# Performance work log

Hardware: AMD Instinct MI355X
Metric: run time of the kernel (lower is better)

The kernel has to match this reference:

```python
import jax, jax.numpy as jnp
import numpy as np
import math

B, C, N, T = 8, 128, 256, 64  # batch, d_model, nodes, timesteps
H = 8                          # attention heads
NUM_STEPS = 50                 # diffusion steps


def _conv2d(x, w, b):
    # Conv2d with kernel (1,3), padding (0,1); x: (B,C,N,T), w: (O,I,1,3)
    y = jax.lax.conv_general_dilated(x, w, (1, 1), [(0, 0), (1, 1)],
                                     dimension_numbers=('NCHW', 'OIHW', 'NCHW'))
    return y + b[None, :, None, None]


def _linear(x, w, b=None):
    y = jnp.einsum('...i,oi->...o', x, w)
    return y if b is None else y + b


def _ln(x, g, b, eps=1e-5):
    m = jnp.mean(x, -1, keepdims=True)
    v = jnp.var(x, -1, keepdims=True)
    return (x - m) * jax.lax.rsqrt(v + eps) * g + b


def _forward(step, x, adj, wq, bq, wk, bk, w1, b1, w2, b2, theta,
             ln0_g, ln0_b, ln1_g, ln1_b, p1_w, p1_b, p2_w, p2_b,
             dxc_w, dxc_b, dec_w, dec_b, dc1_w, dc1_b, dp2_w, dp2_b):
    dk = C // H
    sq = 1.0 / math.sqrt(dk)
    sc = 1.0 / math.sqrt(C)
    # ---- normalized graph Laplacian: D^{-1/2} A D^{-1/2} (get_laplacian, normalize=True)
    d = jnp.sum(adj, -1) ** -0.5
    Lap = adj * d[:, None] * d[None, :]  # (N,N)
    # ---- temporal attention with conv-derived Q/K (MultiHeadAttentionAwareTemporal)
    q = _conv2d(x, wq, bq).reshape(B, H, dk, N, T).transpose(0, 3, 1, 4, 2)  # (B,N,H,T,dk)
    k = _conv2d(x, wk, bk).reshape(B, H, dk, N, T).transpose(0, 3, 1, 4, 2)
    v = _linear(x.transpose(0, 2, 3, 1), w1, b1).reshape(B, N, T, H, dk).transpose(0, 1, 3, 2, 4)
    p = jax.nn.softmax(jnp.einsum('bnhtd,bnhsd->bnhts', q, k) * sq, axis=-1)
    o = jnp.einsum('bnhts,bnhsd->bnhtd', p, v).transpose(0, 1, 3, 2, 4).reshape(B, N, T, C)
    xp = x.transpose(0, 2, 3, 1) + _ln(_linear(o, w2, b2), ln0_g, ln0_b)  # (B,N,T,C)
    # ---- spatial attention GCN (Spatial_Attention_layer + spatialAttentionGCN)
    xt = xp.transpose(0, 2, 1, 3)  # (B,T,N,C)
    sat = jax.nn.softmax(jnp.einsum('btnf,btmf->btnm', xt, xt) * sc, axis=-1) * sc
    y = jnp.einsum('btnm,btmf->btnf', Lap[None, None] * sat, xt)
    y = jax.nn.relu(_linear(y, theta)).transpose(0, 2, 1, 3)  # (B,N,T,C)
    h = xp + _ln(y, ln1_g, ln1_b)
    # ---- diffusion step embedding (DiffusionEmbedding)
    dim = C // 2
    freqs = 10.0 ** (jnp.arange(dim, dtype=jnp.float32) / (dim - 1) * 4.0)
    tab = jnp.arange(NUM_STEPS, dtype=jnp.float32)[:, None] * freqs[None, :]
    tab = jnp.concatenate([jnp.sin(tab), jnp.cos(tab)], -1)  # (NUM_STEPS, C)
    e = jax.nn.silu(_linear(tab[step], p1_w, p1_b))
    e = jax.nn.silu(_linear(e, p2_w, p2_b))  # (B,C)
    h = h + e[:, None, None, :]
    # ---- Decoder: conv + sigmoid-gated add + relu + 1x1 projection to 2 channels
    enc = h.transpose(0, 3, 1, 2)  # (B,C,N,T)
    xh = _conv2d(enc, dxc_w, dxc_b)
    ec = _conv2d(enc, dec_w, dec_b)
    out = jax.nn.relu(xh + jax.nn.sigmoid(ec) + _conv2d(ec, dc1_w, dc1_b))
    out = jnp.einsum('bcnt,oc->bont', out, dp2_w) + dp2_b[None, :, None, None]  # (B,2,N,T)
    return out


def setup_inputs() -> dict:
    key = jax.random.key(0)
    ks = iter(jax.random.split(key, 40))
    s = 1.0 / math.sqrt(C)
    sk = 1.0 / math.sqrt(3 * C)

    def nrm(shape, scale):
        return jax.random.normal(next(ks), shape, jnp.float32) * scale

    return {
        'x': nrm((B, C, N, T), 1.0),
        'adj': jax.random.uniform(next(ks), (N, N), jnp.float32, 0.1, 1.0),
        'step': jax.random.randint(next(ks), (B,), 0, NUM_STEPS, jnp.int32),
        'wq': nrm((C, C, 1, 3), sk), 'bq': jnp.zeros((C,), jnp.float32),
        'wk': nrm((C, C, 1, 3), sk), 'bk': jnp.zeros((C,), jnp.float32),
        'w1': nrm((C, C), s), 'b1': jnp.zeros((C,), jnp.float32),
        'w2': nrm((C, C), s), 'b2': jnp.zeros((C,), jnp.float32),
        'theta': nrm((C, C), s),
        'ln0_g': jnp.ones((C,), jnp.float32), 'ln0_b': jnp.zeros((C,), jnp.float32),
        'ln1_g': jnp.ones((C,), jnp.float32), 'ln1_b': jnp.zeros((C,), jnp.float32),
        'p1_w': nrm((C, C), s), 'p1_b': jnp.zeros((C,), jnp.float32),
        'p2_w': nrm((C, C), s), 'p2_b': jnp.zeros((C,), jnp.float32),
        'dxc_w': nrm((C, C, 1, 3), sk), 'dxc_b': jnp.zeros((C,), jnp.float32),
        'dec_w': nrm((C, C, 1, 3), sk), 'dec_b': jnp.zeros((C,), jnp.float32),
        'dc1_w': nrm((C, C, 1, 3), sk), 'dc1_b': jnp.zeros((C,), jnp.float32),
        'dp2_w': nrm((2, C), s), 'dp2_b': jnp.zeros((2,), jnp.float32),
    }


def reference(x, adj, step, wq, bq, wk, bk, w1, b1, w2, b2, theta,
              ln0_g, ln0_b, ln1_g, ln1_b, p1_w, p1_b, p2_w, p2_b,
              dxc_w, dxc_b, dec_w, dec_b, dc1_w, dc1_b, dp2_w, dp2_b):
    return _forward(step, x, adj, wq, bq, wk, bk, w1, b1, w2, b2, theta,
                    ln0_g, ln0_b, ln1_g, ln1_b, p1_w, p1_b, p2_w, p2_b,
                    dxc_w, dxc_b, dec_w, dec_b, dc1_w, dc1_b, dp2_w, dp2_b)
```

## Files before the change

### kernel.cpp

```cpp
#include <hip/hip_runtime.h>
#include <hip/hip_bf16.h>

namespace {

constexpr int C = 128, N = 256, T = 64, Bsz = 8;
constexpr int TILE = T * C;
constexpr size_t BIGE = (size_t)Bsz * N * T * C;

typedef short v8s __attribute__((ext_vector_type(8)));
typedef float v4f __attribute__((ext_vector_type(4)));

__device__ __forceinline__ float bfu(unsigned short u) {
  unsigned int x = ((unsigned int)u) << 16;
  return __uint_as_float(x);
}
__device__ __forceinline__ unsigned short f2b(float v) {
  __hip_bfloat16 h = __float2bfloat16(v);
  return *(unsigned short*)&h;
}
__device__ __forceinline__ unsigned int pk2(float a, float b) {
  return (unsigned int)f2b(a) | ((unsigned int)f2b(b) << 16);
}
__device__ __forceinline__ float ld(const void* p, size_t i, int f32) {
  if (f32) return ((const float*)p)[i];
  return bfu(((const unsigned short*)p)[i]);
}
__device__ __forceinline__ float sigm(float x) { return 1.f / (1.f + __expf(-x)); }

__global__ __launch_bounds__(64) void k_sniff(const unsigned short* x, int* flag) {
  __shared__ int cnt[64];
  int tid = threadIdx.x;
  int c = 0;
  for (int u = 0; u < 8; ++u) {
    unsigned short v = x[tid * 8 + u];
    int e = (v >> 7) & 255;
    c += (e >= 97 && e <= 157) ? 1 : 0;
  }
  cnt[tid] = c;
  __syncthreads();
  if (tid == 0) {
    int s = 0;
    for (int i = 0; i < 64; ++i) s += cnt[i];
    flag[0] = (s < 435) ? 1 : 0;
  }
}

struct PrepArgs {
  const int* flag;
  const void *wq, *wk, *w1, *w2, *th, *dxc, *dec, *dc1;
  const void *bq, *bk, *b1, *b2, *l0g, *l0b, *l1g, *l1b, *dxcb, *decb, *dc1b, *dp2w, *dp2b;
  unsigned short *wqkB, *w1B, *w2B;
  __hip_bfloat16* thB;
  unsigned short *decWb, *dxcWb, *dc1Wb;
  float *bqk, *b1f, *b2f, *l0gf, *l0bf, *l1gf, *l1bf, *dxcbf, *decbf, *dc1bf, *dp2wf, *dp2bf;
};

__global__ __launch_bounds__(256) void k_prep(PrepArgs a) {
  int f = a.flag[0];
  int idx = blockIdx.x * blockDim.x + threadIdx.x;
  int stride = gridDim.x * blockDim.x;
  for (int i = idx; i < 256 * 384; i += stride) {
    int o = i / 384, k = i - o * 384;
    int j = k >> 7, ii = k & 127;
    float v = (o < 128) ? ld(a.wq, (o * 128 + ii) * 3 + j, f)
                        : ld(a.wk, ((o - 128) * 128 + ii) * 3 + j, f);
    a.wqkB[i] = f2b(v);
  }
  for (int i = idx; i < 16384; i += stride) {
    a.w1B[i] = f2b(ld(a.w1, i, f));
    a.w2B[i] = f2b(ld(a.w2, i, f));
    a.thB[i] = __float2bfloat16(ld(a.th, i, f));
  }
  for (int i = idx; i < 16384; i += stride) {
    int o = i >> 7, ii = i & 127;
    int sbase = (o * 128 + ii) * 3;
#pragma unroll
    for (int j = 0; j < 3; ++j) {
      int dsti = o * 384 + j * 128 + ii;
      a.decWb[dsti] = f2b(ld(a.dec, sbase + j, f));
      a.dxcWb[dsti] = f2b(ld(a.dxc, sbase + j, f));
      a.dc1Wb[dsti] = f2b(ld(a.dc1, sbase + j, f));
    }
  }
  for (int i = idx; i < 256; i += stride) {
    a.bqk[i] = (i < 128) ? ld(a.bq, i, f) : ld(a.bk, i - 128, f);
    a.dp2wf[i] = ld(a.dp2w, i, f);
  }
  for (int i = idx; i < 128; i += stride) {
    a.b1f[i] = ld(a.b1, i, f);   a.b2f[i] = ld(a.b2, i, f);
    a.l0gf[i] = ld(a.l0g, i, f); a.l0bf[i] = ld(a.l0b, i, f);
    a.l1gf[i] = ld(a.l1g, i, f); a.l1bf[i] = ld(a.l1b, i, f);
    a.dxcbf[i] = ld(a.dxcb, i, f); a.decbf[i] = ld(a.decb, i, f); a.dc1bf[i] = ld(a.dc1b, i, f);
  }
  if (idx < 2) a.dp2bf[idx] = ld(a.dp2b, idx, f);
}

__global__ __launch_bounds__(256) void k_lap(const void* adj, const int* flag, float* lap) {
  __shared__ float dsh[256];
  int f = flag[0];
  int tid = threadIdx.x;
  float s = 0.f;
  for (int m = 0; m < 256; ++m) s += ld(adj, tid * 256 + m, f);
  dsh[tid] = 1.f / sqrtf(s);
  __syncthreads();
  for (int idx = tid; idx < 65536; idx += 256) {
    int n = idx >> 8, m = idx & 255;
    lap[idx] = ld(adj, idx, f) * dsh[n] * dsh[m];
  }
}

__global__ __launch_bounds__(128) void k_emb(const int* step, const int* flag,
                                             const void* p1w, const void* p1b,
                                             const void* p2w, const void* p2b, float* e) {
  int b = blockIdx.x, c = threadIdx.x;
  int f = flag[0];
  __shared__ float tab[128], e1[128];
  float sv = (float)step[b];
  int i0 = c & 63;
  float fr = powf(10.f, (float)i0 / 63.f * 4.f);
  float ang = sv * fr;
  tab[c] = (c < 64) ? sinf(ang) : cosf(ang);
  __syncthreads();
  float a = ld(p1b, c, f);
  for (int i = 0; i < 128; ++i) a += tab[i] * ld(p1w, c * 128 + i, f);
  a = a * sigm(a);
  e1[c] = a;
  __syncthreads();
  float a2 = ld(p2b, c, f);
  for (int i = 0; i < 128; ++i) a2 += e1[i] * ld(p2w, c * 128 + i, f);
  e[b * 128 + c] = a2 * sigm(a2);
}

constexpr int XBS = 136;
constexpr int VTS = 72;

__global__ __launch_bounds__(512, 4) void k_mega1(
    const void* xin, const int* flag,
    const unsigned short* wqkB, const float* bqk,
    const unsigned short* w1B, const float* b1f,
    const unsigned short* w2B, const float* b2f,
    const float* l0g, const float* l0b, float* g0) {
  int bn = blockIdx.x, b = bn >> 8, n = bn & 255;
  __shared__ unsigned short Xb[66 * XBS];
  __shared__ unsigned short qo[64 * XBS];
  __shared__ unsigned short kls[64 * XBS];
  __shared__ unsigned short vT[128 * VTS];
  __shared__ float pS[8 * 64], pQ[8 * 64];
  __shared__ float mrow[64], vrow[64];
  int tid = threadIdx.x;
  int wv = tid >> 6, lane = tid & 63, quad = lane >> 4, lr = lane & 15;
  int f = flag[0];
  int hb = wv * 16;
  const v8s zz = {0, 0, 0, 0, 0, 0, 0, 0};
  {
    size_t xoff = (size_t)b * C * N * T + (size_t)n * T;
    for (int idx = tid * 4; idx < TILE; idx += 2048) {
      int i = idx >> 6, t = idx & 63;
      unsigned short pk[4];
      if (f) {
        float4 v4 = *(const float4*)&((const float*)xin)[xoff + (size_t)i * N * T + t];
        pk[0] = f2b(v4.x); pk[1] = f2b(v4.y); pk[2] = f2b(v4.z); pk[3] = f2b(v4.w);
      } else {
        ushort4 u4 = *(const ushort4*)&((const unsigned short*)xin)[xoff + (size_t)i * N * T + t];
        pk[0] = u4.x; pk[1] = u4.y; pk[2] = u4.z; pk[3] = u4.w;
      }
#pragma unroll
      for (int u = 0; u < 4; ++u) Xb[(t + u + 1) * XBS + i] = pk[u];
    }
    if (tid < 128) { Xb[tid] = 0; Xb[65 * XBS + tid] = 0; }
  }
  __syncthreads();
  {
    int mt0 = wv * 2;
    v4f acc[2][4];
#pragma unroll
    for (int mi = 0; mi < 2; ++mi)
#pragma unroll
      for (int nt = 0; nt < 4; ++nt) acc[mi][nt] = (v4f){0.f, 0.f, 0.f, 0.f};
    for (int j = 0; j < 3; ++j) {
#pragma unroll
      for (int kt = 0; kt < 4; ++kt) {
        int ko = j * 128 + kt * 32 + quad * 8;
        v8s a0 = *(const v8s*)&wqkB[(mt0 * 16 + lr) * 384 + ko];
        v8s a1 = *(const v8s*)&wqkB[((mt0 + 1) * 16 + lr) * 384 + ko];
        int bko = kt * 32 + quad * 8;
#pragma unroll
        for (int nt = 0; nt < 4; ++nt) {
          v8s bb = *(const v8s*)&Xb[(nt * 16 + lr + j) * XBS + bko];
          acc[0][nt] = __builtin_amdgcn_mfma_f32_16x16x32_bf16(a0, bb, acc[0][nt], 0, 0, 0);
          acc[1][nt] = __builtin_amdgcn_mfma_f32_16x16x32_bf16(a1, bb, acc[1][nt], 0, 0, 0);
        }
      }
    }
    unsigned short* dst = (wv < 4) ? qo : kls;
#pragma unroll
    for (int mi = 0; mi < 2; ++mi) {
      int og = (mt0 + mi) * 16 + quad * 4;
      int oo = og & 127;
#pragma unroll
      for (int nt = 0; nt < 4; ++nt) {
        int t = nt * 16 + lr;
        *(unsigned int*)&dst[t * XBS + oo] =
            pk2(acc[mi][nt][0] + bqk[og], acc[mi][nt][1] + bqk[og + 1]);
        *(unsigned int*)&dst[t * XBS + oo + 2] =
            pk2(acc[mi][nt][2] + bqk[og + 2], acc[mi][nt][3] + bqk[og + 3]);
      }
    }
  }
  {
    v4f av[4];
#pragma unroll
    for (int nt = 0; nt < 4; ++nt) av[nt] = (v4f){0.f, 0.f, 0.f, 0.f};
#pragma unroll
    for (int kt = 0; kt < 4; ++kt) {
      int ko = kt * 32 + quad * 8;
      v8s a = *(const v8s*)&w1B[(wv * 16 + lr) * 128 + ko];
#pragma unroll
      for (int nt = 0; nt < 4; ++nt) {
        v8s bb = *(const v8s*)&Xb[(nt * 16 + lr + 1) * XBS + ko];
        av[nt] = __builtin_amdgcn_mfma_f32_16x16x32_bf16(a, bb, av[nt], 0, 0, 0);
      }
    }
#pragma unroll
    for (int nt = 0; nt < 4; ++nt) {
      int t = nt * 16 + lr;
#pragma unroll
      for (int r = 0; r < 4; ++r) {
        int o = hb + quad * 4 + r;
        vT[o * VTS + t] = f2b(av[nt][r] + b1f[o]);
      }
    }
  }
  __syncthreads();
  {
    v4f sa[4][4];
#pragma unroll
    for (int ms = 0; ms < 4; ++ms)
#pragma unroll
      for (int nt = 0; nt < 4; ++nt) sa[ms][nt] = (v4f){0.f, 0.f, 0.f, 0.f};
    {
      v8s afs[4], bfs[4];
#pragma unroll
      for (int ms = 0; ms < 4; ++ms)
        afs[ms] = (quad < 2) ? *(const v8s*)&kls[(ms * 16 + lr) * XBS + hb + quad * 8] : zz;
#pragma unroll
      for (int nt = 0; nt < 4; ++nt)
        bfs[nt] = (quad < 2) ? *(const v8s*)&qo[(nt * 16 + lr) * XBS + hb + quad * 8] : zz;
#pragma unroll
      for (int ms = 0; ms < 4; ++ms)
#pragma unroll
        for (int nt = 0; nt < 4; ++nt)
          sa[ms][nt] = __builtin_amdgcn_mfma_f32_16x16x32_bf16(afs[ms], bfs[nt], sa[ms][nt], 0, 0, 0);
    }
#pragma unroll
    for (int nt = 0; nt < 4; ++nt) {
      float mx = -1e30f;
#pragma unroll
      for (int ms = 0; ms < 4; ++ms)
#pragma unroll
        for (int r = 0; r < 4; ++r) {
          float v = sa[ms][nt][r] * 0.25f;
          sa[ms][nt][r] = v;
          mx = fmaxf(mx, v);
        }
      mx = fmaxf(mx, __shfl_xor(mx, 16, 64));
      mx = fmaxf(mx, __shfl_xor(mx, 32, 64));
      float ssum = 0.f;
#pragma unroll
      for (int ms = 0; ms < 4; ++ms)
#pragma unroll
        for (int r = 0; r < 4; ++r) {
          float e = __expf(sa[ms][nt][r] - mx);
          sa[ms][nt][r] = e;
          ssum += e;
        }
      ssum += __shfl_xor(ssum, 16, 64);
      ssum += __shfl_xor(ssum, 32, 64);
      float inv = 1.f / ssum;
#pragma unroll
      for (int ms = 0; ms < 4; ++ms)
#pragma unroll
        for (int r = 0; r < 4; ++r) sa[ms][nt][r] *= inv;
    }
    v4f ov[4];
#pragma unroll
    for (int nt = 0; nt < 4; ++nt) ov[nt] = (v4f){0.f, 0.f, 0.f, 0.f};
#pragma unroll
    for (int kt = 0; kt < 2; ++kt) {
      unsigned int pA[4][2], pB[4][2];
#pragma unroll
      for (int nt = 0; nt < 4; ++nt) {
#pragma unroll
        for (int h = 0; h < 2; ++h) {
          pA[nt][h] = pk2(sa[2 * kt][nt][2 * h], sa[2 * kt][nt][2 * h + 1]);
          pB[nt][h] = pk2(sa[2 * kt + 1][nt][2 * h], sa[2 * kt + 1][nt][2 * h + 1]);
        }
      }
      v8s aV = *(const v8s*)&vT[(hb + lr) * VTS + kt * 32 + quad * 8];
#pragma unroll
      for (int nt = 0; nt < 4; ++nt) {
        union { unsigned int u[4]; v8s s; } bu;
#pragma unroll
        for (int w = 0; w < 4; ++w) {
          int src = (2 * (quad & 1) + (w >> 1)) * 16 + lr;
          unsigned int x0 = (unsigned int)__shfl((int)pA[nt][w & 1], src, 64);
          unsigned int x1 = (unsigned int)__shfl((int)pB[nt][w & 1], src, 64);
          bu.u[w] = (quad >> 1) ? x1 : x0;
        }
        ov[nt] = __builtin_amdgcn_mfma_f32_16x16x32_bf16(aV, bu.s, ov[nt], 0, 0, 0);
      }
    }
#pragma unroll
    for (int nt = 0; nt < 4; ++nt) {
      int t = nt * 16 + lr;
      *(unsigned int*)&qo[t * XBS + hb + quad * 4] = pk2(ov[nt][0], ov[nt][1]);
      *(unsigned int*)&qo[t * XBS + hb + quad * 4 + 2] = pk2(ov[nt][2], ov[nt][3]);
    }
  }
  __syncthreads();
  v4f aw[4];
  {
#pragma unroll
    for (int nt = 0; nt < 4; ++nt) aw[nt] = (v4f){0.f, 0.f, 0.f, 0.f};
#pragma unroll
    for (int kt = 0; kt < 4; ++kt) {
      int ko = kt * 32 + quad * 8;
      v8s a = *(const v8s*)&w2B[(wv * 16 + lr) * 128 + ko];
#pragma unroll
      for (int nt = 0; nt < 4; ++nt) {
        v8s bb = *(const v8s*)&qo[(nt * 16 + lr) * XBS + ko];
        aw[nt] = __builtin_amdgcn_mfma_f32_16x16x32_bf16(a, bb, aw[nt], 0, 0, 0);
      }
    }
    int ob = hb + quad * 4;
#pragma unroll
    for (int nt = 0; nt < 4; ++nt) {
      float s = 0.f, q2 = 0.f;
#pragma unroll
      for (int r = 0; r < 4; ++r) {
        aw[nt][r] += b2f[ob + r];
        s += aw[nt][r];
        q2 += aw[nt][r] * aw[nt][r];
      }
      s += __shfl_xor(s, 16, 64);  s += __shfl_xor(s, 32, 64);
      q2 += __shfl_xor(q2, 16, 64); q2 += __shfl_xor(q2, 32, 64);
      if (quad == 0) {
        pS[wv * 64 + nt * 16 + lr] = s;
        pQ[wv * 64 + nt * 16 + lr] = q2;
      }
    }
  }
  __syncthreads();
  if (tid < 64) {
    float s = 0.f, q2 = 0.f;
#pragma unroll
    for (int w = 0; w < 8; ++w) { s += pS[w * 64 + tid]; q2 += pQ[w * 64 + tid]; }
    float mm = s * (1.f / 128.f);
    mrow[tid] = mm;
    vrow[tid] = rsqrtf(q2 * (1.f / 128.f) - mm * mm + 1e-5f);
  }
  __syncthreads();
  {
    int ob = hb + quad * 4;
    float gg[4], bb2[4];
#pragma unroll
    for (int r = 0; r < 4; ++r) { gg[r] = l0g[ob + r]; bb2[r] = l0b[ob + r]; }
    float* dst = g0 + (size_t)bn * TILE;
#pragma unroll
    for (int nt = 0; nt < 4; ++nt) {
      int t = nt * 16 + lr;
      float m = mrow[t], rs = vrow[t];
      ushort4 xr = *(const ushort4*)&Xb[(t + 1) * XBS + ob];
      float4 o4;
      o4.x = (aw[nt][0] - m) * rs * gg[0] + bb2[0] + bfu(xr.x);
      o4.y = (aw[nt][1] - m) * rs * gg[1] + bb2[1] + bfu(xr.y);
      o4.z = (aw[nt][2] - m) * rs * gg[2] + bb2[2] + bfu(xr.z);
      o4.w = (aw[nt][3] - m) * rs * gg[3] + bb2[3] + bfu(xr.w);
      *(float4*)&dst[t * 128 + ob] = o4;
    }
  }
}

constexpr int XS = 136;
constexpr int TS = 264;

__global__ __launch_bounds__(512, 1) void k_megasp(
    const float* g0, const float* lap, float* yout) {
  int bt = blockIdx.x, b = bt >> 6, t = bt & 63;
  __shared__ unsigned short Xhi[256 * XS];
  __shared__ unsigned short Xlo[256 * XS];
  unsigned short* Xt = Xlo;
  unsigned short* Pld = Xhi;
  int tid = threadIdx.x;
  int wv = tid >> 6, lane = tid & 63, quad = lane >> 4, lr = lane & 15;
  int wrow0 = wv * 32;
  const float sc = 0.08838834764831845f;
  {
    size_t base = (size_t)b * (N * (size_t)TILE) + (size_t)t * 128;
    for (int idx = tid * 4; idx < 32768; idx += 2048) {
      int n = idx >> 7, c = idx & 127;
      float4 v4 = *(const float4*)&g0[base + (size_t)n * TILE + c];
      ushort4 h, l;
      h.x = f2b(v4.x); l.x = f2b(v4.x - bfu(h.x));
      h.y = f2b(v4.y); l.y = f2b(v4.y - bfu(h.y));
      h.z = f2b(v4.z); l.z = f2b(v4.z - bfu(h.z));
      h.w = f2b(v4.w); l.w = f2b(v4.w - bfu(h.w));
      *(ushort4*)&Xhi[n * XS + c] = h;
      *(ushort4*)&Xlo[n * XS + c] = l;
    }
  }
  __syncthreads();
  v4f acc[2][16];
#pragma unroll
  for (int mi = 0; mi < 2; ++mi)
#pragma unroll
    for (int nt = 0; nt < 16; ++nt) acc[mi][nt] = (v4f){0.f, 0.f, 0.f, 0.f};
  for (int kt = 0; kt < 4; ++kt) {
    int ko = kt * 32 + quad * 8;
    v8s ah0 = *(const v8s*)&Xhi[(wrow0 + lr) * XS + ko];
    v8s al0 = *(const v8s*)&Xlo[(wrow0 + lr) * XS + ko];
    v8s ah1 = *(const v8s*)&Xhi[(wrow0 + 16 + lr) * XS + ko];
    v8s al1 = *(const v8s*)&Xlo[(wrow0 + 16 + lr) * XS + ko];
#pragma unroll
    for (int nt = 0; nt < 16; ++nt) {
      v8s bh = *(const v8s*)&Xhi[(nt * 16 + lr) * XS + ko];
      v8s bl = *(const v8s*)&Xlo[(nt * 16 + lr) * XS + ko];
      acc[0][nt] = __builtin_amdgcn_mfma_f32_16x16x32_bf16(ah0, bh, acc[0][nt], 0, 0, 0);
      acc[0][nt] = __builtin_amdgcn_mfma_f32_16x16x32_bf16(ah0, bl, acc[0][nt], 0, 0, 0);
      acc[0][nt] = __builtin_amdgcn_mfma_f32_16x16x32_bf16(al0, bh, acc[0][nt], 0, 0, 0);
      acc[1][nt] = __builtin_amdgcn_mfma_f32_16x16x32_bf16(ah1, bh, acc[1][nt], 0, 0, 0);
      acc[1][nt] = __builtin_amdgcn_mfma_f32_16x16x32_bf16(ah1, bl, acc[1][nt], 0, 0, 0);
      acc[1][nt] = __builtin_amdgcn_mfma_f32_16x16x32_bf16(al1, bh, acc[1][nt], 0, 0, 0);
    }
  }
  __syncthreads();
  for (int task = tid; task < 8192; task += 512) {
    int c = task & 127, n0 = (task >> 7) * 4;
    ushort4 w;
    w.x = Xhi[(n0 + 0) * XS + c];
    w.y = Xhi[(n0 + 1) * XS + c];
    w.z = Xhi[(n0 + 2) * XS + c];
    w.w = Xhi[(n0 + 3) * XS + c];
    *(ushort4*)&Xt[c * TS + n0] = w;
  }
  __syncthreads();
  unsigned int pk1[2][8][2];
#pragma unroll
  for (int mi = 0; mi < 2; ++mi) {
#pragma unroll
    for (int r = 0; r < 4; ++r) {
      int row = wrow0 + 16 * mi + quad * 4 + r;
      float mx = -1e30f;
#pragma unroll
      for (int nt = 0; nt < 16; ++nt) {
        acc[mi][nt][r] *= sc;
        mx = fmaxf(mx, acc[mi][nt][r]);
      }
#pragma unroll
      for (int m = 8; m > 0; m >>= 1) mx = fmaxf(mx, __shfl_xor(mx, m, 16));
      float ex[16];
      float ssum = 0.f;
#pragma unroll
      for (int nt = 0; nt < 16; ++nt) { ex[nt] = __expf(acc[mi][nt][r] - mx); ssum += ex[nt]; }
#pragma unroll
      for (int m = 8; m > 0; m >>= 1) ssum += __shfl_xor(ssum, m, 16);
      float inv = sc / ssum;
      const float* lrow = lap + row * 256 + lr;
#pragma unroll
      for (int nt = 0; nt < 8; ++nt)
        Pld[row * XS + nt * 16 + lr] = f2b(ex[nt] * inv * lrow[nt * 16]);
#pragma unroll
      for (int nt = 8; nt < 16; ++nt) {
        unsigned int hbw = (unsigned int)f2b(ex[nt] * inv * lrow[nt * 16]);
        if ((r & 1) == 0) pk1[mi][nt - 8][r >> 1] = hbw;
        else pk1[mi][nt - 8][r >> 1] |= hbw << 16;
      }
    }
  }
  v4f acc2[2][8];
#pragma unroll
  for (int mi = 0; mi < 2; ++mi)
#pragma unroll
    for (int nt = 0; nt < 8; ++nt) acc2[mi][nt] = (v4f){0.f, 0.f, 0.f, 0.f};
#pragma unroll
  for (int h = 0; h < 2; ++h) {
    if (h == 1) {
#pragma unroll
      for (int mi = 0; mi < 2; ++mi) {
        int rowb = wrow0 + 16 * mi + quad * 4;
#pragma unroll
        for (int k = 0; k < 8; ++k) {
          int col = k * 16 + lr;
          unsigned int u0 = pk1[mi][k][0], u1 = pk1[mi][k][1];
          Pld[(rowb + 0) * XS + col] = (unsigned short)u0;
          Pld[(rowb + 1) * XS + col] = (unsigned short)(u0 >> 16);
          Pld[(rowb + 2) * XS + col] = (unsigned short)u1;
          Pld[(rowb + 3) * XS + col] = (unsigned short)(u1 >> 16);
        }
      }
    }
    for (int kt = 0; kt < 4; ++kt) {
      int ko = kt * 32 + quad * 8;
      v8s pa0 = *(const v8s*)&Pld[(wrow0 + lr) * XS + ko];
      v8s pa1 = *(const v8s*)&Pld[(wrow0 + 16 + lr) * XS + ko];
#pragma unroll
      for (int nt = 0; nt < 8; ++nt) {
        v8s xb = *(const v8s*)&Xt[(nt * 16 + lr) * TS + h * 128 + ko];
        acc2[0][nt] = __builtin_amdgcn_mfma_f32_16x16x32_bf16(pa0, xb, acc2[0][nt], 0, 0, 0);
        acc2[1][nt] = __builtin_amdgcn_mfma_f32_16x16x32_bf16(pa1, xb, acc2[1][nt], 0, 0, 0);
      }
    }
  }
  float* yb = yout + (size_t)bt * 32768;
#pragma unroll
  for (int mi = 0; mi < 2; ++mi) {
    int nb = wrow0 + 16 * mi + quad * 4;
#pragma unroll
    for (int nt = 0; nt < 8; ++nt) {
      int c = nt * 16 + lr;
#pragma unroll
      for (int r = 0; r < 4; ++r)
        yb[(size_t)(nb + r) * 128 + c] = acc2[mi][nt][r];
    }
  }
}

__global__ __launch_bounds__(512, 4) void k_theta(
    const float* y, const unsigned short* thB, float* g0,
    const float* l1g, const float* l1b, const float* e) {
  int bt = blockIdx.x, b = bt >> 6, t = bt & 63;
  __shared__ unsigned short ths[128 * 136];
  __shared__ unsigned short yh[64 * 136], yl[64 * 136];
  __shared__ float pS[8][64], pQ[8][64];
  __shared__ float mrow[64], vrow[64];
  int tid = threadIdx.x;
  int wv = tid >> 6, lane = tid & 63, quad = lane >> 4, lr = lane & 15;
  int ob = wv * 16 + quad * 4;
  for (int idx = tid * 8; idx < 16384; idx += 4096) {
    int o = idx >> 7, k = idx & 127;
    *(uint4*)&ths[o * 136 + k] = *(const uint4*)&thB[idx];
  }
  const float* eb = e + b * 128;
  float gg[4], bb2[4], ev[4];
#pragma unroll
  for (int r = 0; r < 4; ++r) {
    gg[r] = l1g[ob + r]; bb2[r] = l1b[ob + r]; ev[r] = eb[ob + r];
  }
  const float* ybase = y + (size_t)bt * 32768;
  __syncthreads();
  for (int chunk = 0; chunk < 4; ++chunk) {
    int n0 = chunk * 64;
    for (int idx = tid * 4; idx < 8192; idx += 2048) {
      int rr = idx >> 7, c = idx & 127;
      float4 v4 = *(const float4*)&ybase[(size_t)(n0 + rr) * 128 + c];
      ushort4 h, l;
      h.x = f2b(v4.x); l.x = f2b(v4.x - bfu(h.x));
      h.y = f2b(v4.y); l.y = f2b(v4.y - bfu(h.y));
      h.z = f2b(v4.z); l.z = f2b(v4.z - bfu(h.z));
      h.w = f2b(v4.w); l.w = f2b(v4.w - bfu(h.w));
      *(ushort4*)&yh[rr * 136 + c] = h;
      *(ushort4*)&yl[rr * 136 + c] = l;
    }
    __syncthreads();
    v4f acc[4];
#pragma unroll
    for (int nt = 0; nt < 4; ++nt) acc[nt] = (v4f){0.f, 0.f, 0.f, 0.f};
#pragma unroll
    for (int kt = 0; kt < 4; ++kt) {
      int ko = kt * 32 + quad * 8;
      v8s a = *(const v8s*)&ths[(wv * 16 + lr) * 136 + ko];
#pragma unroll
      for (int nt = 0; nt < 4; ++nt) {
        v8s bh = *(const v8s*)&yh[(nt * 16 + lr) * 136 + ko];
        v8s bl = *(const v8s*)&yl[(nt * 16 + lr) * 136 + ko];
        acc[nt] = __builtin_amdgcn_mfma_f32_16x16x32_bf16(a, bh, acc[nt], 0, 0, 0);
        acc[nt] = __builtin_amdgcn_mfma_f32_16x16x32_bf16(a, bl, acc[nt], 0, 0, 0);
      }
    }
#pragma unroll
    for (int nt = 0; nt < 4; ++nt) {
      float s = 0.f, q2 = 0.f;
#pragma unroll
      for (int r = 0; r < 4; ++r) {
        float v = fmaxf(acc[nt][r], 0.f);
        acc[nt][r] = v;
        s += v; q2 += v * v;
      }
      s += __shfl_xor(s, 16, 64);  s += __shfl_xor(s, 32, 64);
      q2 += __shfl_xor(q2, 16, 64); q2 += __shfl_xor(q2, 32, 64);
      if (quad == 0) { pS[wv][nt * 16 + lr] = s; pQ[wv][nt * 16 + lr] = q2; }
    }
    __syncthreads();
    if (tid < 64) {
      float s = 0.f, q2 = 0.f;
#pragma unroll
      for (int w = 0; w < 8; ++w) { s += pS[w][tid]; q2 += pQ[w][tid]; }
      float mm = s * (1.f / 128.f);
      mrow[tid] = mm;
      vrow[tid] = rsqrtf(q2 * (1.f / 128.f) - mm * mm + 1e-5f);
    }
    __syncthreads();
#pragma unroll
    for (int nt = 0; nt < 4; ++nt) {
      int nn = nt * 16 + lr;
      int n = n0 + nn;
      float m = mrow[nn], rs = vrow[nn];
      size_t ga = ((size_t)(b * 256 + n)) * TILE + (size_t)t * 128 + ob;
      float4 xa = *(const float4*)&g0[ga];
      float4 h0;
      h0.x = (acc[nt][0] - m) * rs * gg[0] + bb2[0] + xa.x + ev[0];
      h0.y = (acc[nt][1] - m) * rs * gg[1] + bb2[1] + xa.y + ev[1];
      h0.z = (acc[nt][2] - m) * rs * gg[2] + bb2[2] + xa.z + ev[2];
      h0.w = (acc[nt][3] - m) * rs * gg[3] + bb2[3] + xa.w + ev[3];
      *(float4*)&g0[ga] = h0;
    }
    __syncthreads();
  }
}

__global__ __launch_bounds__(512, 4) void k_megadec(
    const float* g0, const unsigned short* decW, const float* decb,
    const unsigned short* dxcW, const float* dxcb,
    const unsigned short* dc1W, const float* dc1b,
    const float* dp2w, const float* dp2b, const int* flag, void* outv) {
  int bn = blockIdx.x, b = bn >> 8, n = bn & 255;
  int f32o = flag[0];
  __shared__ unsigned short Xm[66 * XBS];
  __shared__ unsigned short E2[66 * XBS];
  __shared__ float pb0[8][64], pb1[8][64];
  int tid = threadIdx.x;
  int wv = tid >> 6, lane = tid & 63, quad = lane >> 4, lr = lane & 15;
  int m0 = wv * 16;
  const float* gp = g0 + (size_t)bn * TILE;
  for (int idx = tid * 4; idx < TILE; idx += 2048) {
    int t = idx >> 7, c = idx & 127;
    float4 v4 = *(const float4*)&gp[idx];
    ushort4 pk;
    pk.x = f2b(v4.x); pk.y = f2b(v4.y); pk.z = f2b(v4.z); pk.w = f2b(v4.w);
    *(ushort4*)&Xm[(t + 1) * XBS + c] = pk;
  }
  if (tid < 128) {
    Xm[tid] = 0; Xm[65 * XBS + tid] = 0;
    E2[tid] = 0; E2[65 * XBS + tid] = 0;
  }
  __syncthreads();
  v4f acc[4];
  float ecv[4][4];
#pragma unroll
  for (int nt = 0; nt < 4; ++nt) acc[nt] = (v4f){0.f, 0.f, 0.f, 0.f};
  for (int j = 0; j < 3; ++j) {
#pragma unroll
    for (int kt = 0; kt < 4; ++kt) {
      v8s a = *(const v8s*)&decW[(m0 + lr) * 384 + j * 128 + kt * 32 + quad * 8];
      int bko = kt * 32 + quad * 8;
#pragma unroll
      for (int nt = 0; nt < 4; ++nt) {
        v8s bb = *(const v8s*)&Xm[(nt * 16 + lr + j) * XBS + bko];
        acc[nt] = __builtin_amdgcn_mfma_f32_16x16x32_bf16(a, bb, acc[nt], 0, 0, 0);
      }
    }
  }
#pragma unroll
  for (int nt = 0; nt < 4; ++nt) {
    int t = nt * 16 + lr;
    int o = m0 + quad * 4;
    ushort4 pk;
#pragma unroll
    for (int r = 0; r < 4; ++r) {
      float v = acc[nt][r] + decb[o + r];
      ecv[nt][r] = v;
      ((unsigned short*)&pk)[r] = f2b(v);
    }
    *(ushort4*)&E2[(t + 1) * XBS + o] = pk;
  }
  __syncthreads();
  v4f ax[4], ac[4];
#pragma unroll
  for (int nt = 0; nt < 4; ++nt) { ax[nt] = (v4f){0.f,0.f,0.f,0.f}; ac[nt] = (v4f){0.f,0.f,0.f,0.f}; }
  for (int j = 0; j < 3; ++j) {
#pragma unroll
    for (int kt = 0; kt < 4; ++kt) {
      int wo = (m0 + lr) * 384 + j * 128 + kt * 32 + quad * 8;
      v8s a1 = *(const v8s*)&dxcW[wo];
      v8s a2 = *(const v8s*)&dc1W[wo];
      int bko = kt * 32 + quad * 8;
#pragma unroll
      for (int nt = 0; nt < 4; ++nt) {
        int row = (nt * 16 + lr + j) * XBS + bko;
        v8s b1 = *(const v8s*)&Xm[row];
        v8s b2v = *(const v8s*)&E2[row];
        ax[nt] = __builtin_amdgcn_mfma_f32_16x16x32_bf16(a1, b1, ax[nt], 0, 0, 0);
        ac[nt] = __builtin_amdgcn_mfma_f32_16x16x32_bf16(a2, b2v, ac[nt], 0, 0, 0);
      }
    }
  }
#pragma unroll
  for (int nt = 0; nt < 4; ++nt) {
    float p0 = 0.f, p1 = 0.f;
#pragma unroll
    for (int r = 0; r < 4; ++r) {
      int o = m0 + quad * 4 + r;
      float v = fmaxf(ax[nt][r] + dxcb[o] + sigm(ecv[nt][r]) + ac[nt][r] + dc1b[o], 0.f);
      p0 += v * dp2w[o];
      p1 += v * dp2w[128 + o];
    }
    p0 += __shfl_xor(p0, 16, 64); p0 += __shfl_xor(p0, 32, 64);
    p1 += __shfl_xor(p1, 16, 64); p1 += __shfl_xor(p1, 32, 64);
    if (quad == 0) { pb0[wv][nt * 16 + lr] = p0; pb1[wv][nt * 16 + lr] = p1; }
  }
  __syncthreads();
  if (tid < 128) {
    int ch = tid >> 6, t = tid & 63;
    float s = 0.f;
    if (ch == 0) { for (int w = 0; w < 8; ++w) s += pb0[w][t]; s += dp2b[0]; }
    else         { for (int w = 0; w < 8; ++w) s += pb1[w][t]; s += dp2b[1]; }
    size_t oi = ((size_t)(b * 2 + ch) * 256 + n) * 64 + t;
    if (f32o) ((float*)outv)[oi] = s;
    else ((__hip_bfloat16*)outv)[oi] = __float2bfloat16(s);
  }
}

}

extern "C" void kernel_launch(void* const* d_in, const int* in_sizes, int n_in,
                              void* d_out, int out_size, void* d_ws, size_t ws_size,
                              hipStream_t stream) {
  (void)in_sizes; (void)n_in; (void)out_size; (void)ws_size;
  const void* x    = d_in[0];
  const void* adj  = d_in[1];
  const int*  step = (const int*)d_in[2];
  const void* wq   = d_in[3];
  const void* bq   = d_in[4];
  const void* wk   = d_in[5];
  const void* bk   = d_in[6];
  const void* w1   = d_in[7];
  const void* b1   = d_in[8];
  const void* w2   = d_in[9];
  const void* b2   = d_in[10];
  const void* th   = d_in[11];
  const void* l0g  = d_in[12];
  const void* l0b  = d_in[13];
  const void* l1g  = d_in[14];
  const void* l1b  = d_in[15];
  const void* p1w  = d_in[16];
  const void* p1b  = d_in[17];
  const void* p2w  = d_in[18];
  const void* p2b  = d_in[19];
  const void* dxcw = d_in[20];
  const void* dxcb = d_in[21];
  const void* decw = d_in[22];
  const void* decb = d_in[23];
  const void* dc1w = d_in[24];
  const void* dc1b = d_in[25];
  const void* dp2w = d_in[26];
  const void* dp2b = d_in[27];

  float* ws = (float*)d_ws;
  int* flag = (int*)ws;
  float* p = ws + 16;
  float* e     = p; p += 1024;
  float* lap   = p; p += 65536;
  float* wqkBv = p; p += 49152;
  float* w1Bv  = p; p += 8192;
  float* w2Bv  = p; p += 8192;
  float* thBv  = p; p += 8192;
  float* decWv = p; p += 24576;
  float* dxcWv = p; p += 24576;
  float* dc1Wv = p; p += 24576;
  float* bqk   = p; p += 256;
  float* b1f   = p; p += 128;
  float* b2f   = p; p += 128;
  float* l0gf  = p; p += 128;
  float* l0bf  = p; p += 128;
  float* l1gf  = p; p += 128;
  float* l1bf  = p; p += 128;
  float* dxcbf = p; p += 128;
  float* decbf = p; p += 128;
  float* dc1bf = p; p += 128;
  float* dp2wf = p; p += 256;
  float* dp2bf = p; p += 8;
  size_t off = (size_t)(p - ws);
  off = (off + 127) & ~(size_t)127;
  float* xf = ws + off;
  float* g0 = xf + BIGE;

  PrepArgs pa;
  pa.flag = flag;
  pa.wq = wq; pa.wk = wk; pa.w1 = w1; pa.w2 = w2; pa.th = th;
  pa.dxc = dxcw; pa.dec = decw; pa.dc1 = dc1w;
  pa.bq = bq; pa.bk = bk; pa.b1 = b1; pa.b2 = b2;
  pa.l0g = l0g; pa.l0b = l0b; pa.l1g = l1g; pa.l1b = l1b;
  pa.dxcb = dxcb; pa.decb = decb; pa.dc1b = dc1b; pa.dp2w = dp2w; pa.dp2b = dp2b;
  pa.wqkB = (unsigned short*)wqkBv;
  pa.w1B = (unsigned short*)w1Bv;
  pa.w2B = (unsigned short*)w2Bv;
  pa.thB = (__hip_bfloat16*)thBv;
  pa.decWb = (unsigned short*)decWv;
  pa.dxcWb = (unsigned short*)dxcWv;
  pa.dc1Wb = (unsigned short*)dc1Wv;
  pa.bqk = bqk; pa.b1f = b1f; pa.b2f = b2f;
  pa.l0gf = l0gf; pa.l0bf = l0bf; pa.l1gf = l1gf; pa.l1bf = l1bf;
  pa.dxcbf = dxcbf; pa.decbf = decbf; pa.dc1bf = dc1bf; pa.dp2wf = dp2wf; pa.dp2bf = dp2bf;

  k_sniff<<<1, 64, 0, stream>>>((const unsigned short*)x, flag);
  k_prep<<<128, 256, 0, stream>>>(pa);
  k_lap<<<1, 256, 0, stream>>>(adj, flag, lap);
  k_emb<<<8, 128, 0, stream>>>(step, flag, p1w, p1b, p2w, p2b, e);

  k_mega1<<<2048, 512, 0, stream>>>(x, flag, (const unsigned short*)wqkBv, bqk,
                                    (const unsigned short*)w1Bv, b1f,
                                    (const unsigned short*)w2Bv, b2f, l0gf, l0bf, g0);
  k_megasp<<<512, 512, 0, stream>>>(g0, lap, xf);
  k_theta<<<512, 512, 0, stream>>>(xf, (const unsigned short*)thBv, g0, l1gf, l1bf, e);
  k_megadec<<<2048, 512, 0, stream>>>(g0, (const unsigned short*)decWv, decbf,
                                      (const unsigned short*)dxcWv, dxcbf,
                                      (const unsigned short*)dc1Wv, dc1bf,
                                      dp2wf, dp2bf, flag, d_out);
}
```

Measured before the change: 495.2 us.

## Fuse theta projection into spatial kernel, merge prep kernels, pass bf16 intermediate

Merges the prep, Laplacian and embedding kernels into one launch, splitting the Laplacian across 64 blocks. Fuses the theta linear, ReLU, LayerNorm and residual/embedding add into the spatial attention kernel, so the fp32 y intermediate is no longer written to and re-read from global memory. The fused result is stored as bf16 for the decoder kernel, halving that traffic and removing its conversion step. The cost is lower precision, since the theta input drops from hi/lo split to plain bf16, plus higher register pressure (16 accumulator tiles) in a kernel limited to one block per SM.

```diff
diff --git a/kernel.cpp b/kernel.cpp
--- a/kernel.cpp
+++ b/kernel.cpp
@@ -55,80 +55,83 @@
   float *bqk, *b1f, *b2f, *l0gf, *l0bf, *l1gf, *l1bf, *dxcbf, *decbf, *dc1bf, *dp2wf, *dp2bf;
 };
 
-__global__ __launch_bounds__(256) void k_prep(PrepArgs a) {
+__global__ __launch_bounds__(256) void k_prepall(
+    PrepArgs a, const void* adj, float* lap, const int* step,
+    const void* p1w, const void* p1b, const void* p2w, const void* p2b, float* e) {
+  __shared__ float sh[256];
+  __shared__ float e1[128];
   int f = a.flag[0];
-  int idx = blockIdx.x * blockDim.x + threadIdx.x;
-  int stride = gridDim.x * blockDim.x;
-  for (int i = idx; i < 256 * 384; i += stride) {
-    int o = i / 384, k = i - o * 384;
-    int j = k >> 7, ii = k & 127;
-    float v = (o < 128) ? ld(a.wq, (o * 128 + ii) * 3 + j, f)
-                        : ld(a.wk, ((o - 128) * 128 + ii) * 3 + j, f);
-    a.wqkB[i] = f2b(v);
-  }
-  for (int i = idx; i < 16384; i += stride) {
-    a.w1B[i] = f2b(ld(a.w1, i, f));
-    a.w2B[i] = f2b(ld(a.w2, i, f));
-    a.thB[i] = __float2bfloat16(ld(a.th, i, f));
-  }
-  for (int i = idx; i < 16384; i += stride) {
-    int o = i >> 7, ii = i & 127;
-    int sbase = (o * 128 + ii) * 3;
-#pragma unroll
-    for (int j = 0; j < 3; ++j) {
-      int dsti = o * 384 + j * 128 + ii;
-      a.decWb[dsti] = f2b(ld(a.dec, sbase + j, f));
-      a.dxcWb[dsti] = f2b(ld(a.dxc, sbase + j, f));
-      a.dc1Wb[dsti] = f2b(ld(a.dc1, sbase + j, f));
-    }
-  }
-  for (int i = idx; i < 256; i += stride) {
-    a.bqk[i] = (i < 128) ? ld(a.bq, i, f) : ld(a.bk, i - 128, f);
-    a.dp2wf[i] = ld(a.dp2w, i, f);
-  }
-  for (int i = idx; i < 128; i += stride) {
-    a.b1f[i] = ld(a.b1, i, f);   a.b2f[i] = ld(a.b2, i, f);
-    a.l0gf[i] = ld(a.l0g, i, f); a.l0bf[i] = ld(a.l0b, i, f);
-    a.l1gf[i] = ld(a.l1g, i, f); a.l1bf[i] = ld(a.l1b, i, f);
-    a.dxcbf[i] = ld(a.dxcb, i, f); a.decbf[i] = ld(a.decb, i, f); a.dc1bf[i] = ld(a.dc1b, i, f);
-  }
-  if (idx < 2) a.dp2bf[idx] = ld(a.dp2b, idx, f);
-}
-
-__global__ __launch_bounds__(256) void k_lap(const void* adj, const int* flag, float* lap) {
-  __shared__ float dsh[256];
-  int f = flag[0];
-  int tid = threadIdx.x;
-  float s = 0.f;
-  for (int m = 0; m < 256; ++m) s += ld(adj, tid * 256 + m, f);
-  dsh[tid] = 1.f / sqrtf(s);
-  __syncthreads();
-  for (int idx = tid; idx < 65536; idx += 256) {
-    int n = idx >> 8, m = idx & 255;
-    lap[idx] = ld(adj, idx, f) * dsh[n] * dsh[m];
-  }
-}
-
-__global__ __launch_bounds__(128) void k_emb(const int* step, const int* flag,
-                                             const void* p1w, const void* p1b,
-                                             const void* p2w, const void* p2b, float* e) {
-  int b = blockIdx.x, c = threadIdx.x;
-  int f = flag[0];
-  __shared__ float tab[128], e1[128];
-  float sv = (float)step[b];
-  int i0 = c & 63;
-  float fr = powf(10.f, (float)i0 / 63.f * 4.f);
-  float ang = sv * fr;
-  tab[c] = (c < 64) ? sinf(ang) : cosf(ang);
-  __syncthreads();
-  float a = ld(p1b, c, f);
-  for (int i = 0; i < 128; ++i) a += tab[i] * ld(p1w, c * 128 + i, f);
-  a = a * sigm(a);
-  e1[c] = a;
-  __syncthreads();
-  float a2 = ld(p2b, c, f);
-  for (int i = 0; i < 128; ++i) a2 += e1[i] * ld(p2w, c * 128 + i, f);
-  e[b * 128 + c] = a2 * sigm(a2);
+  int blk = blockIdx.x, tid = threadIdx.x;
+  if (blk < 128) {
+    int idx = blk * 256 + tid;
+    const int stride = 32768;
+    for (int i = idx; i < 256 * 384; i += stride) {
+      int o = i / 384, k = i - o * 384;
+      int j = k >> 7, ii = k & 127;
+      float v = (o < 128) ? ld(a.wq, (o * 128 + ii) * 3 + j, f)
+                          : ld(a.wk, ((o - 128) * 128 + ii) * 3 + j, f);
+      a.wqkB[i] = f2b(v);
+    }
+    for (int i = idx; i < 16384; i += stride) {
+      a.w1B[i] = f2b(ld(a.w1, i, f));
+      a.w2B[i] = f2b(ld(a.w2, i, f));
+      a.thB[i] = __float2bfloat16(ld(a.th, i, f));
+    }
+    for (int i = idx; i < 16384; i += stride) {
+      int o = i >> 7, ii = i & 127;
+      int sbase = (o * 128 + ii) * 3;
+#pragma unroll
+      for (int j = 0; j < 3; ++j) {
+        int dsti = o * 384 + j * 128 + ii;
+        a.decWb[dsti] = f2b(ld(a.dec, sbase + j, f));
+        a.dxcWb[dsti] = f2b(ld(a.dxc, sbase + j, f));
+        a.dc1Wb[dsti] = f2b(ld(a.dc1, sbase + j, f));
+      }
+    }
+    for (int i = idx; i < 256; i += stride) {
+      a.bqk[i] = (i < 128) ? ld(a.bq, i, f) : ld(a.bk, i - 128, f);
+      a.dp2wf[i] = ld(a.dp2w, i, f);
+    }
+    for (int i = idx; i < 128; i += stride) {
+      a.b1f[i] = ld(a.b1, i, f);   a.b2f[i] = ld(a.b2, i, f);
+      a.l0gf[i] = ld(a.l0g, i, f); a.l0bf[i] = ld(a.l0b, i, f);
+      a.l1gf[i] = ld(a.l1g, i, f); a.l1bf[i] = ld(a.l1b, i, f);
+      a.dxcbf[i] = ld(a.dxcb, i, f); a.decbf[i] = ld(a.decb, i, f); a.dc1bf[i] = ld(a.dc1b, i, f);
+    }
+    if (idx < 2) a.dp2bf[idx] = ld(a.dp2b, idx, f);
+  } else if (blk < 192) {
+    float s = 0.f;
+    for (int m = 0; m < 256; ++m) s += ld(adj, tid * 256 + m, f);
+    sh[tid] = 1.f / sqrtf(s);
+    __syncthreads();
+    int n0 = (blk - 128) * 4;
+    for (int idx = tid; idx < 1024; idx += 256) {
+      int n = n0 + (idx >> 8), m = idx & 255;
+      lap[n * 256 + m] = ld(adj, n * 256 + m, f) * sh[n] * sh[m];
+    }
+  } else {
+    int b = blk - 192;
+    if (tid < 128) {
+      float sv = (float)step[b];
+      int i0 = tid & 63;
+      float fr = powf(10.f, (float)i0 / 63.f * 4.f);
+      float ang = sv * fr;
+      sh[tid] = (tid < 64) ? sinf(ang) : cosf(ang);
+    }
+    __syncthreads();
+    if (tid < 128) {
+      float aa = ld(p1b, tid, f);
+      for (int i = 0; i < 128; ++i) aa += sh[i] * ld(p1w, tid * 128 + i, f);
+      aa = aa * sigm(aa);
+      e1[tid] = aa;
+    }
+    __syncthreads();
+    if (tid < 128) {
+      float a2 = ld(p2b, tid, f);
+      for (int i = 0; i < 128; ++i) a2 += e1[i] * ld(p2w, tid * 128 + i, f);
+      e[b * 128 + tid] = a2 * sigm(a2);
+    }
+  }
 }
 
 constexpr int XBS = 136;
@@ -385,12 +388,17 @@
 constexpr int TS = 264;
 
 __global__ __launch_bounds__(512, 1) void k_megasp(
-    const float* g0, const float* lap, float* yout) {
+    const float* g0, const float* lap, const unsigned short* thB,
+    const float* l1g, const float* l1b, const float* e, unsigned short* g0b) {
   int bt = blockIdx.x, b = bt >> 6, t = bt & 63;
-  __shared__ unsigned short Xhi[256 * XS];
-  __shared__ unsigned short Xlo[256 * XS];
-  unsigned short* Xt = Xlo;
-  unsigned short* Pld = Xhi;
+  __shared__ unsigned short R1[256 * XS];
+  __shared__ unsigned short R2[256 * XS];
+  __shared__ float pS[8][256], pQ[8][256];
+  __shared__ float mrow[256], vrow[256];
+  unsigned short* Xhi = R1;
+  unsigned short* Xlo = R2;
+  unsigned short* Xt = R2;
+  unsigned short* Pld = R1;
   int tid = threadIdx.x;
   int wv = tid >> 6, lane = tid & 63, quad = lane >> 4, lr = lane & 15;
   int wrow0 = wv * 32;
@@ -511,7 +519,9 @@
       }
     }
   }
-  float* yb = yout + (size_t)bt * 32768;
+  __syncthreads();
+  unsigned short* yB = R2;
+  unsigned short* ths = R1;
 #pragma unroll
   for (int mi = 0; mi < 2; ++mi) {
     int nb = wrow0 + 16 * mi + quad * 4;
@@ -520,106 +530,74 @@
       int c = nt * 16 + lr;
 #pragma unroll
       for (int r = 0; r < 4; ++r)
-        yb[(size_t)(nb + r) * 128 + c] = acc2[mi][nt][r];
-    }
-  }
-}
-
-__global__ __launch_bounds__(512, 4) void k_theta(
-    const float* y, const unsigned short* thB, float* g0,
-    const float* l1g, const float* l1b, const float* e) {
-  int bt = blockIdx.x, b = bt >> 6, t = bt & 63;
-  __shared__ unsigned short ths[128 * 136];
-  __shared__ unsigned short yh[64 * 136], yl[64 * 136];
-  __shared__ float pS[8][64], pQ[8][64];
-  __shared__ float mrow[64], vrow[64];
-  int tid = threadIdx.x;
-  int wv = tid >> 6, lane = tid & 63, quad = lane >> 4, lr = lane & 15;
-  int ob = wv * 16 + quad * 4;
+        yB[(nb + r) * XS + c] = f2b(acc2[mi][nt][r]);
+    }
+  }
   for (int idx = tid * 8; idx < 16384; idx += 4096) {
     int o = idx >> 7, k = idx & 127;
     *(uint4*)&ths[o * 136 + k] = *(const uint4*)&thB[idx];
   }
-  const float* eb = e + b * 128;
-  float gg[4], bb2[4], ev[4];
-#pragma unroll
-  for (int r = 0; r < 4; ++r) {
-    gg[r] = l1g[ob + r]; bb2[r] = l1b[ob + r]; ev[r] = eb[ob + r];
-  }
-  const float* ybase = y + (size_t)bt * 32768;
-  __syncthreads();
-  for (int chunk = 0; chunk < 4; ++chunk) {
-    int n0 = chunk * 64;
-    for (int idx = tid * 4; idx < 8192; idx += 2048) {
-      int rr = idx >> 7, c = idx & 127;
-      float4 v4 = *(const float4*)&ybase[(size_t)(n0 + rr) * 128 + c];
-      ushort4 h, l;
-      h.x = f2b(v4.x); l.x = f2b(v4.x - bfu(h.x));
-      h.y = f2b(v4.y); l.y = f2b(v4.y - bfu(h.y));
-      h.z = f2b(v4.z); l.z = f2b(v4.z - bfu(h.z));
-      h.w = f2b(v4.w); l.w = f2b(v4.w - bfu(h.w));
-      *(ushort4*)&yh[rr * 136 + c] = h;
-      *(ushort4*)&yl[rr * 136 + c] = l;
-    }
-    __syncthreads();
-    v4f acc[4];
-#pragma unroll
-    for (int nt = 0; nt < 4; ++nt) acc[nt] = (v4f){0.f, 0.f, 0.f, 0.f};
-#pragma unroll
-    for (int kt = 0; kt < 4; ++kt) {
-      int ko = kt * 32 + quad * 8;
-      v8s a = *(const v8s*)&ths[(wv * 16 + lr) * 136 + ko];
-#pragma unroll
-      for (int nt = 0; nt < 4; ++nt) {
-        v8s bh = *(const v8s*)&yh[(nt * 16 + lr) * 136 + ko];
-        v8s bl = *(const v8s*)&yl[(nt * 16 + lr) * 136 + ko];
-        acc[nt] = __builtin_amdgcn_mfma_f32_16x16x32_bf16(a, bh, acc[nt], 0, 0, 0);
-        acc[nt] = __builtin_amdgcn_mfma_f32_16x16x32_bf16(a, bl, acc[nt], 0, 0, 0);
-      }
-    }
-#pragma unroll
-    for (int nt = 0; nt < 4; ++nt) {
-      float s = 0.f, q2 = 0.f;
-#pragma unroll
-      for (int r = 0; r < 4; ++r) {
-        float v = fmaxf(acc[nt][r], 0.f);
-        acc[nt][r] = v;
-        s += v; q2 += v * v;
-      }
-      s += __shfl_xor(s, 16, 64);  s += __shfl_xor(s, 32, 64);
-      q2 += __shfl_xor(q2, 16, 64); q2 += __shfl_xor(q2, 32, 64);
-      if (quad == 0) { pS[wv][nt * 16 + lr] = s; pQ[wv][nt * 16 + lr] = q2; }
-    }
-    __syncthreads();
-    if (tid < 64) {
-      float s = 0.f, q2 = 0.f;
-#pragma unroll
-      for (int w = 0; w < 8; ++w) { s += pS[w][tid]; q2 += pQ[w][tid]; }
-      float mm = s * (1.f / 128.f);
-      mrow[tid] = mm;
-      vrow[tid] = rsqrtf(q2 * (1.f / 128.f) - mm * mm + 1e-5f);
-    }
-    __syncthreads();
-#pragma unroll
-    for (int nt = 0; nt < 4; ++nt) {
-      int nn = nt * 16 + lr;
-      int n = n0 + nn;
-      float m = mrow[nn], rs = vrow[nn];
-      size_t ga = ((size_t)(b * 256 + n)) * TILE + (size_t)t * 128 + ob;
+  __syncthreads();
+  v4f acc3[16];
+#pragma unroll
+  for (int nt = 0; nt < 16; ++nt) acc3[nt] = (v4f){0.f, 0.f, 0.f, 0.f};
+#pragma unroll
+  for (int kt = 0; kt < 4; ++kt) {
+    int ko = kt * 32 + quad * 8;
+    v8s a = *(const v8s*)&ths[(wv * 16 + lr) * 136 + ko];
+#pragma unroll
+    for (int nt = 0; nt < 16; ++nt) {
+      v8s bb = *(const v8s*)&yB[(nt * 16 + lr) * XS + ko];
+      acc3[nt] = __builtin_amdgcn_mfma_f32_16x16x32_bf16(a, bb, acc3[nt], 0, 0, 0);
+    }
+  }
+#pragma unroll
+  for (int nt = 0; nt < 16; ++nt) {
+    float s = 0.f, q2 = 0.f;
+#pragma unroll
+    for (int r = 0; r < 4; ++r) {
+      float v = fmaxf(acc3[nt][r], 0.f);
+      acc3[nt][r] = v;
+      s += v; q2 += v * v;
+    }
+    s += __shfl_xor(s, 16, 64);  s += __shfl_xor(s, 32, 64);
+    q2 += __shfl_xor(q2, 16, 64); q2 += __shfl_xor(q2, 32, 64);
+    if (quad == 0) { pS[wv][nt * 16 + lr] = s; pQ[wv][nt * 16 + lr] = q2; }
+  }
+  __syncthreads();
+  if (tid < 256) {
+    float s = 0.f, q2 = 0.f;
+#pragma unroll
+    for (int w = 0; w < 8; ++w) { s += pS[w][tid]; q2 += pQ[w][tid]; }
+    float mm = s * (1.f / 128.f);
+    mrow[tid] = mm;
+    vrow[tid] = rsqrtf(q2 * (1.f / 128.f) - mm * mm + 1e-5f);
+  }
+  __syncthreads();
+  {
+    int o0 = wv * 16 + quad * 4;
+    float gg[4], bb2[4], ev[4];
+    const float* eb = e + b * 128;
+#pragma unroll
+    for (int r = 0; r < 4; ++r) { gg[r] = l1g[o0 + r]; bb2[r] = l1b[o0 + r]; ev[r] = eb[o0 + r]; }
+#pragma unroll
+    for (int nt = 0; nt < 16; ++nt) {
+      int n = nt * 16 + lr;
+      float m = mrow[n], rs = vrow[n];
+      size_t ga = ((size_t)(b * 256 + n)) * TILE + (size_t)t * 128 + o0;
       float4 xa = *(const float4*)&g0[ga];
-      float4 h0;
-      h0.x = (acc[nt][0] - m) * rs * gg[0] + bb2[0] + xa.x + ev[0];
-      h0.y = (acc[nt][1] - m) * rs * gg[1] + bb2[1] + xa.y + ev[1];
-      h0.z = (acc[nt][2] - m) * rs * gg[2] + bb2[2] + xa.z + ev[2];
-      h0.w = (acc[nt][3] - m) * rs * gg[3] + bb2[3] + xa.w + ev[3];
-      *(float4*)&g0[ga] = h0;
-    }
-    __syncthreads();
+      ushort4 pk;
+      pk.x = f2b((acc3[nt][0] - m) * rs * gg[0] + bb2[0] + xa.x + ev[0]);
+      pk.y = f2b((acc3[nt][1] - m) * rs * gg[1] + bb2[1] + xa.y + ev[1]);
+      pk.z = f2b((acc3[nt][2] - m) * rs * gg[2] + bb2[2] + xa.z + ev[2]);
+      pk.w = f2b((acc3[nt][3] - m) * rs * gg[3] + bb2[3] + xa.w + ev[3]);
+      *(ushort4*)&g0b[ga] = pk;
+    }
   }
 }
 
 __global__ __launch_bounds__(512, 4) void k_megadec(
-    const float* g0, const unsigned short* decW, const float* decb,
+    const unsigned short* g0b, const unsigned short* decW, const float* decb,
     const unsigned short* dxcW, const float* dxcb,
     const unsigned short* dc1W, const float* dc1b,
     const float* dp2w, const float* dp2b, const int* flag, void* outv) {
@@ -631,13 +609,10 @@
   int tid = threadIdx.x;
   int wv = tid >> 6, lane = tid & 63, quad = lane >> 4, lr = lane & 15;
   int m0 = wv * 16;
-  const float* gp = g0 + (size_t)bn * TILE;
-  for (int idx = tid * 4; idx < TILE; idx += 2048) {
+  const unsigned short* gp = g0b + (size_t)bn * TILE;
+  for (int idx = tid * 8; idx < TILE; idx += 4096) {
     int t = idx >> 7, c = idx & 127;
-    float4 v4 = *(const float4*)&gp[idx];
-    ushort4 pk;
-    pk.x = f2b(v4.x); pk.y = f2b(v4.y); pk.z = f2b(v4.z); pk.w = f2b(v4.w);
-    *(ushort4*)&Xm[(t + 1) * XBS + c] = pk;
+    *(uint4*)&Xm[(t + 1) * XBS + c] = *(const uint4*)&gp[idx];
   }
   if (tid < 128) {
     Xm[tid] = 0; Xm[65 * XBS + tid] = 0;
@@ -783,6 +758,7 @@
   off = (off + 127) & ~(size_t)127;
   float* xf = ws + off;
   float* g0 = xf + BIGE;
+  unsigned short* g0b = (unsigned short*)xf;
 
   PrepArgs pa;
   pa.flag = flag;
@@ -803,16 +779,14 @@
   pa.dxcbf = dxcbf; pa.decbf = decbf; pa.dc1bf = dc1bf; pa.dp2wf = dp2wf; pa.dp2bf = dp2bf;
 
   k_sniff<<<1, 64, 0, stream>>>((const unsigned short*)x, flag);
-  k_prep<<<128, 256, 0, stream>>>(pa);
-  k_lap<<<1, 256, 0, stream>>>(adj, flag, lap);
-  k_emb<<<8, 128, 0, stream>>>(step, flag, p1w, p1b, p2w, p2b, e);
+  k_prepall<<<200, 256, 0, stream>>>(pa, adj, lap, step, p1w, p1b, p2w, p2b, e);
 
   k_mega1<<<2048, 512, 0, stream>>>(x, flag, (const unsigned short*)wqkBv, bqk,
                                     (const unsigned short*)w1Bv, b1f,
                                     (const unsigned short*)w2Bv, b2f, l0gf, l0bf, g0);
-  k_megasp<<<512, 512, 0, stream>>>(g0, lap, xf);
-  k_theta<<<512, 512, 0, stream>>>(xf, (const unsigned short*)thBv, g0, l1gf, l1bf, e);
-  k_megadec<<<2048, 512, 0, stream>>>(g0, (const unsigned short*)decWv, decbf,
+  k_megasp<<<512, 512, 0, stream>>>(g0, lap, (const unsigned short*)thBv,
+                                    l1gf, l1bf, e, g0b);
+  k_megadec<<<2048, 512, 0, stream>>>(g0b, (const unsigned short*)decWv, decbf,
                                       (const unsigned short*)dxcWv, dxcbf,
                                       (const unsigned short*)dc1Wv, dc1bf,
                                       dp2wf, dp2bf, flag, d_out);
```

New measurement: 411.1 us. 1.2x faster.
